# Performance work log

Hardware: AMD Instinct MI355X
Metric: run time of the kernel (lower is better)

Reference implementation:

```python
import jax, jax.numpy as jnp
import numpy as np

B, S, D, H = 2, 2048, 1024, 16
DK = D // H


def setup_inputs() -> dict:
    key = jax.random.key(0)
    ks = jax.random.split(key, 12)
    lim = 1.0 / np.sqrt(D)
    def lin(kw, kb):
        W = jax.random.uniform(kw, (D, D), jnp.float32, -lim, lim)
        b = jax.random.uniform(kb, (D,), jnp.float32, -lim, lim)
        return W, b
    Wq, bq = lin(ks[0], ks[1])
    Wk, bk = lin(ks[2], ks[3])
    Wv, bv = lin(ks[4], ks[5])
    Wo, bo = lin(ks[6], ks[7])
    Q = jax.random.normal(ks[8], (B, S, D), jnp.float32)
    K = jax.random.normal(ks[9], (B, S, D), jnp.float32)
    V = jax.random.normal(ks[10], (B, S, D), jnp.float32)
    # causal mask, broadcastable to (B, H, S, S)
    mask = jnp.broadcast_to(jnp.tril(jnp.ones((S, S), jnp.bool_))[None, None], (B, 1, S, S))
    return {"Q": Q, "K": K, "V": V, "mask": mask,
            "Wq": Wq, "bq": bq, "Wk": Wk, "bk": bk,
            "Wv": Wv, "bv": bv, "Wo": Wo, "bo": bo}


def reference(Q, K, V, mask, Wq, bq, Wk, bk, Wv, bv, Wo, bo):
    def split(x):  # (B,S,D) -> (B,H,S,DK)
        return x.reshape(B, S, H, DK).transpose(0, 2, 1, 3)
    q = split(Q @ Wq.T + bq)
    k = split(K @ Wk.T + bk)
    v = split(V @ Wv.T + bv)
    scores = jnp.einsum('bhqd,bhkd->bhqk', q, k) / jnp.sqrt(jnp.float32(DK))
    scores = jnp.where(mask, scores, jnp.float32(-1e9))
    probs = jax.nn.softmax(scores, axis=-1)
    out = jnp.einsum('bhqk,bhkd->bhqd', probs, v)  # (B,H,S,DK)
    out = out.transpose(0, 2, 1, 3).reshape(B, S, D)
    return out @ Wo.T + bo
```

## Files before the change

### kernel.cpp

```cpp
#include <hip/hip_runtime.h>

#define S_LEN 2048
#define D_DIM 1024
#define H_NUM 16
#define DK_DIM 64
#define BATCH 2
#define M_TOT (BATCH * S_LEN)

typedef __bf16 bf16x8 __attribute__((ext_vector_type(8)));
typedef float f32x4 __attribute__((ext_vector_type(4)));
typedef unsigned short u16;

__device__ inline u16 f2bf(float f) {
  union { float f; unsigned u; } v; v.f = f;
  unsigned u = v.u;
  return (u16)((u + 0x7FFFu + ((u >> 16) & 1u)) >> 16);
}

__global__ __launch_bounds__(256)
void proj_kernel(const float* __restrict__ Q, const float* __restrict__ K,
                 const float* __restrict__ V,
                 const float* __restrict__ Wq, const float* __restrict__ bq,
                 const float* __restrict__ Wk, const float* __restrict__ bk,
                 const float* __restrict__ Wv, const float* __restrict__ bv,
                 u16* __restrict__ qh, u16* __restrict__ kh,
                 u16* __restrict__ vt) {
  const int z = blockIdx.z;
  const float* X    = (z == 0) ? Q  : (z == 1) ? K  : V;
  const float* W    = (z == 0) ? Wq : (z == 1) ? Wk : Wv;
  const float* bias = (z == 0) ? bq : (z == 1) ? bk : bv;
  u16* out          = (z == 0) ? qh : (z == 1) ? kh : vt;

  __shared__ __align__(16) u16 Asm[128][40];
  __shared__ __align__(16) u16 Bsm[128][40];

  const int tid  = threadIdx.x;
  const int m0   = blockIdx.x * 128;
  const int n0   = blockIdx.y * 128;
  const int wid  = tid >> 6;
  const int lane = tid & 63;
  const int col  = lane & 15;
  const int quad = lane >> 4;
  const int wm   = (wid >> 1) * 64;
  const int wn   = (wid & 1) * 64;

  f32x4 acc[4][4];
  const f32x4 zero4 = {0.f, 0.f, 0.f, 0.f};
  for (int i = 0; i < 4; i++)
    for (int j = 0; j < 4; j++) acc[i][j] = zero4;

  const int sr = tid >> 3;
  const int sc = (tid & 7) * 4;

  for (int k0 = 0; k0 < D_DIM; k0 += 32) {
    __syncthreads();
    for (int p = 0; p < 4; p++) {
      const int row = p * 32 + sr;
      const float4 av = *reinterpret_cast<const float4*>(
          &X[(size_t)(m0 + row) * D_DIM + k0 + sc]);
      ushort4 aw;
      aw.x = f2bf(av.x); aw.y = f2bf(av.y); aw.z = f2bf(av.z); aw.w = f2bf(av.w);
      *reinterpret_cast<ushort4*>(&Asm[row][sc]) = aw;
      const float4 bvv = *reinterpret_cast<const float4*>(
          &W[(size_t)(n0 + row) * D_DIM + k0 + sc]);
      ushort4 bw;
      bw.x = f2bf(bvv.x); bw.y = f2bf(bvv.y); bw.z = f2bf(bvv.z); bw.w = f2bf(bvv.w);
      *reinterpret_cast<ushort4*>(&Bsm[row][sc]) = bw;
    }
    __syncthreads();

    bf16x8 af[4], bfm[4];
    for (int i = 0; i < 4; i++)
      af[i] = *reinterpret_cast<const bf16x8*>(&Asm[wm + i * 16 + col][quad * 8]);
    for (int j = 0; j < 4; j++)
      bfm[j] = *reinterpret_cast<const bf16x8*>(&Bsm[wn + j * 16 + col][quad * 8]);
    for (int i = 0; i < 4; i++)
      for (int j = 0; j < 4; j++)
        acc[i][j] = __builtin_amdgcn_mfma_f32_16x16x32_bf16(af[i], bfm[j],
                                                            acc[i][j], 0, 0, 0);
  }

  for (int i = 0; i < 4; i++) {
    const int gm_base = m0 + wm + i * 16 + quad * 4;
    for (int j = 0; j < 4; j++) {
      const int gn = n0 + wn + j * 16 + col;
      const float bb = bias[gn];
      const int h = gn >> 6, dk = gn & 63;
      for (int r = 0; r < 4; r++) {
        const int token = gm_base + r;
        const int b = token >> 11, s = token & (S_LEN - 1);
        const float val = acc[i][j][r] + bb;
        size_t idx;
        if (z == 2)
          idx = ((size_t)(b * H_NUM + h) * DK_DIM + dk) * S_LEN + s;
        else
          idx = ((size_t)(b * H_NUM + h) * S_LEN + s) * DK_DIM + dk;
        out[idx] = f2bf(val);
      }
    }
  }
}

#define SCALE_LOG2 0.18033688f

__global__ __launch_bounds__(256)
void attn_kernel(const u16* __restrict__ qh, const u16* __restrict__ kh,
                 const u16* __restrict__ vt, u16* __restrict__ ctx) {
  __shared__ __align__(16) u16 Ksm[64][72];
  __shared__ __align__(16) u16 Vsm[64][72];
  __shared__ __align__(16) u16 Psm[4][32][72];

  const int tid  = threadIdx.x;
  const int bh   = blockIdx.y;
  const int qb   = (blockIdx.y & 16) ? (15 - blockIdx.x) : blockIdx.x;
  const int q0   = qb * 128;
  const int wid  = tid >> 6;
  const int lane = tid & 63;
  const int col  = lane & 15;
  const int quad = lane >> 4;
  const int qrow_w = q0 + wid * 32;

  bf16x8 qB[2][2];
  for (int ss = 0; ss < 2; ss++) {
    const u16* qp =
        &qh[((size_t)bh * S_LEN + qrow_w + ss * 16 + col) * DK_DIM + quad * 8];
    qB[ss][0] = *reinterpret_cast<const bf16x8*>(qp);
    qB[ss][1] = *reinterpret_cast<const bf16x8*>(qp + 32);
  }

  float m_[2] = {-INFINITY, -INFINITY};
  float l_[2] = {0.f, 0.f};
  f32x4 o[4][2];
  const f32x4 zero4 = {0.f, 0.f, 0.f, 0.f};
  for (int dm = 0; dm < 4; dm++)
    for (int ss = 0; ss < 2; ss++) o[dm][ss] = zero4;

  const int ntiles = qb * 2 + 2;
  const int sr = tid >> 2;
  const int sc = (tid & 3) * 8;

  for (int t = 0; t < ntiles; t++) {
    const int kv0 = t * 64;
    __syncthreads();
    {
      const u16* kp = &kh[((size_t)bh * S_LEN + kv0 + sr) * DK_DIM + sc];
      *reinterpret_cast<uint4*>(&Ksm[sr][sc]) =
          *reinterpret_cast<const uint4*>(kp);
      *reinterpret_cast<uint4*>(&Ksm[sr][sc + 32]) =
          *reinterpret_cast<const uint4*>(kp + 32);
      const u16* vp = &vt[((size_t)bh * DK_DIM + sr) * S_LEN + kv0 + sc];
      *reinterpret_cast<uint4*>(&Vsm[sr][sc]) =
          *reinterpret_cast<const uint4*>(vp);
      *reinterpret_cast<uint4*>(&Vsm[sr][sc + 32]) =
          *reinterpret_cast<const uint4*>(vp + 32);
    }
    __syncthreads();

    bf16x8 kA[4][2];
    for (int nc = 0; nc < 4; nc++) {
      kA[nc][0] = *reinterpret_cast<const bf16x8*>(&Ksm[nc * 16 + col][quad * 8]);
      kA[nc][1] =
          *reinterpret_cast<const bf16x8*>(&Ksm[nc * 16 + col][32 + quad * 8]);
    }

    for (int ss = 0; ss < 2; ss++) {
      const int qrs = qrow_w + ss * 16;
      const int qg  = qrs + col;
      f32x4 s[4];
      for (int nc = 0; nc < 4; nc++) {
        f32x4 acc = zero4;
        acc = __builtin_amdgcn_mfma_f32_16x16x32_bf16(kA[nc][0], qB[ss][0],
                                                      acc, 0, 0, 0);
        acc = __builtin_amdgcn_mfma_f32_16x16x32_bf16(kA[nc][1], qB[ss][1],
                                                      acc, 0, 0, 0);
        s[nc] = acc;
      }
      float x[4][4];
      const bool domask = (kv0 + 63 > qrs);
      for (int nc = 0; nc < 4; nc++)
        for (int r = 0; r < 4; r++) {
          float v = s[nc][r] * SCALE_LOG2;
          if (domask && (kv0 + nc * 16 + quad * 4 + r > qg)) v = -INFINITY;
          x[nc][r] = v;
        }
      float tm = x[0][0];
      for (int nc = 0; nc < 4; nc++)
        for (int r = 0; r < 4; r++) tm = fmaxf(tm, x[nc][r]);
      tm = fmaxf(tm, __shfl_xor(tm, 16));
      tm = fmaxf(tm, __shfl_xor(tm, 32));
      const float mn    = fmaxf(m_[ss], tm);
      const float alpha = __builtin_amdgcn_exp2f(m_[ss] - mn);
      m_[ss] = mn;
      float rs = 0.f;
      ushort4 pk[4];
      for (int nc = 0; nc < 4; nc++) {
        float p0 = __builtin_amdgcn_exp2f(x[nc][0] - mn);
        float p1 = __builtin_amdgcn_exp2f(x[nc][1] - mn);
        float p2 = __builtin_amdgcn_exp2f(x[nc][2] - mn);
        float p3 = __builtin_amdgcn_exp2f(x[nc][3] - mn);
        rs += (p0 + p1) + (p2 + p3);
        pk[nc].x = f2bf(p0); pk[nc].y = f2bf(p1);
        pk[nc].z = f2bf(p2); pk[nc].w = f2bf(p3);
      }
      rs += __shfl_xor(rs, 16);
      rs += __shfl_xor(rs, 32);
      l_[ss] = l_[ss] * alpha + rs;
      for (int dm = 0; dm < 4; dm++) o[dm][ss] *= alpha;
      for (int nc = 0; nc < 4; nc++)
        *reinterpret_cast<ushort4*>(
            &Psm[wid][ss * 16 + col][nc * 16 + quad * 4]) = pk[nc];
    }

    asm volatile("s_waitcnt lgkmcnt(0)" ::: "memory");

    bf16x8 pB[2][2];
    for (int ss = 0; ss < 2; ss++) {
      pB[0][ss] = *reinterpret_cast<const bf16x8*>(
          &Psm[wid][ss * 16 + col][quad * 8]);
      pB[1][ss] = *reinterpret_cast<const bf16x8*>(
          &Psm[wid][ss * 16 + col][32 + quad * 8]);
    }
    for (int dm = 0; dm < 4; dm++) {
      const bf16x8 vA0 =
          *reinterpret_cast<const bf16x8*>(&Vsm[dm * 16 + col][quad * 8]);
      const bf16x8 vA1 =
          *reinterpret_cast<const bf16x8*>(&Vsm[dm * 16 + col][32 + quad * 8]);
      for (int ss = 0; ss < 2; ss++) {
        o[dm][ss] = __builtin_amdgcn_mfma_f32_16x16x32_bf16(vA0, pB[0][ss],
                                                            o[dm][ss], 0, 0, 0);
        o[dm][ss] = __builtin_amdgcn_mfma_f32_16x16x32_bf16(vA1, pB[1][ss],
                                                            o[dm][ss], 0, 0, 0);
      }
    }
  }

  const int b = bh >> 4, h = bh & 15;
  for (int ss = 0; ss < 2; ss++) {
    const float inv = 1.0f / l_[ss];
    const int qg = qrow_w + ss * 16 + col;
    for (int dm = 0; dm < 4; dm++) {
      ushort4 w;
      w.x = f2bf(o[dm][ss][0] * inv);
      w.y = f2bf(o[dm][ss][1] * inv);
      w.z = f2bf(o[dm][ss][2] * inv);
      w.w = f2bf(o[dm][ss][3] * inv);
      *reinterpret_cast<ushort4*>(
          &ctx[((size_t)b * S_LEN + qg) * D_DIM + h * DK_DIM + dm * 16 +
               quad * 4]) = w;
    }
  }
}

__global__ __launch_bounds__(256)
void outproj_kernel(const u16* __restrict__ ctx, const float* __restrict__ Wo,
                    const float* __restrict__ bo, float* __restrict__ out) {
  __shared__ __align__(16) u16 Asm[128][40];
  __shared__ __align__(16) u16 Bsm[128][40];

  const int tid  = threadIdx.x;
  const int m0   = blockIdx.x * 128;
  const int n0   = blockIdx.y * 128;
  const int wid  = tid >> 6;
  const int lane = tid & 63;
  const int col  = lane & 15;
  const int quad = lane >> 4;
  const int wm   = (wid >> 1) * 64;
  const int wn   = (wid & 1) * 64;

  f32x4 acc[4][4];
  const f32x4 zero4 = {0.f, 0.f, 0.f, 0.f};
  for (int i = 0; i < 4; i++)
    for (int j = 0; j < 4; j++) acc[i][j] = zero4;

  const int ar = tid >> 2, ac = (tid & 3) * 8;
  const int sr = tid >> 3, sc = (tid & 7) * 4;

  for (int k0 = 0; k0 < D_DIM; k0 += 32) {
    __syncthreads();
    for (int p = 0; p < 2; p++) {
      const int row = p * 64 + ar;
      *reinterpret_cast<uint4*>(&Asm[row][ac]) =
          *reinterpret_cast<const uint4*>(&ctx[(size_t)(m0 + row) * D_DIM + k0 + ac]);
    }
    for (int p = 0; p < 4; p++) {
      const int row = p * 32 + sr;
      const float4 bvv = *reinterpret_cast<const float4*>(
          &Wo[(size_t)(n0 + row) * D_DIM + k0 + sc]);
      ushort4 bw;
      bw.x = f2bf(bvv.x); bw.y = f2bf(bvv.y); bw.z = f2bf(bvv.z); bw.w = f2bf(bvv.w);
      *reinterpret_cast<ushort4*>(&Bsm[row][sc]) = bw;
    }
    __syncthreads();

    bf16x8 af[4], bfm[4];
    for (int i = 0; i < 4; i++)
      af[i] = *reinterpret_cast<const bf16x8*>(&Asm[wm + i * 16 + col][quad * 8]);
    for (int j = 0; j < 4; j++)
      bfm[j] = *reinterpret_cast<const bf16x8*>(&Bsm[wn + j * 16 + col][quad * 8]);
    for (int i = 0; i < 4; i++)
      for (int j = 0; j < 4; j++)
        acc[i][j] = __builtin_amdgcn_mfma_f32_16x16x32_bf16(af[i], bfm[j],
                                                            acc[i][j], 0, 0, 0);
  }

  for (int i = 0; i < 4; i++) {
    const int gm_base = m0 + wm + i * 16 + quad * 4;
    for (int j = 0; j < 4; j++) {
      const int gn = n0 + wn + j * 16 + col;
      const float bb = bo[gn];
      for (int r = 0; r < 4; r++) {
        const int token = gm_base + r;
        out[(size_t)token * D_DIM + gn] = acc[i][j][r] + bb;
      }
    }
  }
}

extern "C" void kernel_launch(void* const* d_in, const int* in_sizes, int n_in,
                              void* d_out, int out_size, void* d_ws,
                              size_t ws_size, hipStream_t stream) {
  const float* Q  = (const float*)d_in[0];
  const float* K  = (const float*)d_in[1];
  const float* V  = (const float*)d_in[2];
  const float* Wq = (const float*)d_in[4];
  const float* bq = (const float*)d_in[5];
  const float* Wk = (const float*)d_in[6];
  const float* bk = (const float*)d_in[7];
  const float* Wv = (const float*)d_in[8];
  const float* bv = (const float*)d_in[9];
  const float* Wo = (const float*)d_in[10];
  const float* bo = (const float*)d_in[11];
  float* out = (float*)d_out;

  const size_t NE = (size_t)BATCH * H_NUM * S_LEN * DK_DIM;
  u16* qh  = (u16*)d_ws;
  u16* kh  = qh + NE;
  u16* vt  = kh + NE;
  u16* ctx = vt + NE;

  proj_kernel<<<dim3(M_TOT / 128, D_DIM / 128, 3), 256, 0, stream>>>(
      Q, K, V, Wq, bq, Wk, bk, Wv, bv, qh, kh, vt);
  attn_kernel<<<dim3(S_LEN / 128, BATCH * H_NUM), 256, 0, stream>>>(qh, kh, vt,
                                                                    ctx);
  outproj_kernel<<<dim3(M_TOT / 128, D_DIM / 128), 256, 0, stream>>>(ctx, Wo,
                                                                     bo, out);
}
```

Measured before the change: 290.9 us.

## Pre-convert inputs to bf16 and use direct-to-LDS loads in projection GEMMs

Adds a separate conversion kernel that casts Q/K/V and all four weight matrices to bf16 once, so the GEMMs no longer convert fp32 per tile. The projection and output GEMMs become one templated kernel. It loads tiles with global_load_lds into an XOR-swizzled 64-wide K tile, swaps MFMA operand order where needed so stores can be vectorized, and writes ushort4/float4 epilogues. This trades an extra full pass over the inputs and extra workspace for cheaper, wider GEMM staging with fewer syncs per K step.

After: 266.4 us. 8.4% less time.

```diff
diff --git a/kernel.cpp b/kernel.cpp
--- a/kernel.cpp
+++ b/kernel.cpp
@@ -6,6 +6,8 @@
 #define DK_DIM 64
 #define BATCH 2
 #define M_TOT (BATCH * S_LEN)
+#define XSZ 4194304
+#define WSZ 1048576
 
 typedef __bf16 bf16x8 __attribute__((ext_vector_type(8)));
 typedef float f32x4 __attribute__((ext_vector_type(4)));
@@ -17,85 +19,161 @@
   return (u16)((u + 0x7FFFu + ((u >> 16) & 1u)) >> 16);
 }
 
+typedef const __attribute__((address_space(1))) unsigned int gu32;
+typedef __attribute__((address_space(3))) unsigned int lu32;
+__device__ inline void glds16(const u16* g, u16* l) {
+  __builtin_amdgcn_global_load_lds((gu32*)g, (lu32*)l, 16, 0, 0);
+}
+
 __global__ __launch_bounds__(256)
-void proj_kernel(const float* __restrict__ Q, const float* __restrict__ K,
-                 const float* __restrict__ V,
-                 const float* __restrict__ Wq, const float* __restrict__ bq,
-                 const float* __restrict__ Wk, const float* __restrict__ bk,
-                 const float* __restrict__ Wv, const float* __restrict__ bv,
-                 u16* __restrict__ qh, u16* __restrict__ kh,
-                 u16* __restrict__ vt) {
-  const int z = blockIdx.z;
-  const float* X    = (z == 0) ? Q  : (z == 1) ? K  : V;
-  const float* W    = (z == 0) ? Wq : (z == 1) ? Wk : Wv;
-  const float* bias = (z == 0) ? bq : (z == 1) ? bk : bv;
-  u16* out          = (z == 0) ? qh : (z == 1) ? kh : vt;
-
-  __shared__ __align__(16) u16 Asm[128][40];
-  __shared__ __align__(16) u16 Bsm[128][40];
-
-  const int tid  = threadIdx.x;
-  const int m0   = blockIdx.x * 128;
-  const int n0   = blockIdx.y * 128;
-  const int wid  = tid >> 6;
-  const int lane = tid & 63;
-  const int col  = lane & 15;
-  const int quad = lane >> 4;
-  const int wm   = (wid >> 1) * 64;
-  const int wn   = (wid & 1) * 64;
+void convert_kernel(const float* __restrict__ Q, const float* __restrict__ K,
+                    const float* __restrict__ V, const float* __restrict__ Wq,
+                    const float* __restrict__ Wk, const float* __restrict__ Wv,
+                    const float* __restrict__ Wo, u16* __restrict__ Xb,
+                    u16* __restrict__ Wb) {
+  const size_t e = ((size_t)blockIdx.x * 256 + threadIdx.x) * 8;
+  const float* src;
+  u16* dst;
+  size_t off;
+  if (e < 3ull * XSZ) {
+    const int a = (int)(e >> 22);
+    src = (a == 0) ? Q : (a == 1) ? K : V;
+    off = e - ((size_t)a << 22);
+    dst = Xb + e;
+  } else {
+    const size_t ew = e - 3ull * XSZ;
+    const int a = (int)(ew >> 20);
+    src = (a == 0) ? Wq : (a == 1) ? Wk : (a == 2) ? Wv : Wo;
+    off = ew - ((size_t)a << 20);
+    dst = Wb + ew;
+  }
+  const float4 v0 = *reinterpret_cast<const float4*>(&src[off]);
+  const float4 v1 = *reinterpret_cast<const float4*>(&src[off + 4]);
+  ushort4 w0, w1;
+  w0.x = f2bf(v0.x); w0.y = f2bf(v0.y); w0.z = f2bf(v0.z); w0.w = f2bf(v0.w);
+  w1.x = f2bf(v1.x); w1.y = f2bf(v1.y); w1.z = f2bf(v1.z); w1.w = f2bf(v1.w);
+  *reinterpret_cast<ushort4*>(dst) = w0;
+  *reinterpret_cast<ushort4*>(dst + 4) = w1;
+}
+
+template <int MODE>
+__global__ __launch_bounds__(256)
+void gemm_kernel(const u16* __restrict__ A0, const u16* __restrict__ B0,
+                 const float* __restrict__ bias0, void* __restrict__ out0,
+                 const u16* __restrict__ A1, const u16* __restrict__ B1,
+                 const float* __restrict__ bias1, void* __restrict__ out1) {
+  const u16* A = A0;
+  const u16* Bw = B0;
+  const float* bias = bias0;
+  void* outp = out0;
+  if (MODE == 0 && blockIdx.z == 1) { A = A1; Bw = B1; bias = bias1; outp = out1; }
+
+  __shared__ __align__(16) u16 Asm[128 * 64];
+  __shared__ __align__(16) u16 Bsm[128 * 64];
+
+  const int tid = threadIdx.x;
+  const int m0 = blockIdx.x * 128, n0 = blockIdx.y * 128;
+  const int wid = tid >> 6, lane = tid & 63;
+  const int col = lane & 15, quad = lane >> 4;
+  const int wm = (wid >> 1) * 64, wn = (wid & 1) * 64;
+
+  const int lr = lane >> 3;
+  const int lc = (lane & 7) ^ lr;
+  const u16* gA = A + (size_t)(m0 + 32 * wid + lr) * D_DIM + lc * 8;
+  const u16* gB = Bw + (size_t)(n0 + 32 * wid + lr) * D_DIM + lc * 8;
 
   f32x4 acc[4][4];
   const f32x4 zero4 = {0.f, 0.f, 0.f, 0.f};
   for (int i = 0; i < 4; i++)
     for (int j = 0; j < 4; j++) acc[i][j] = zero4;
 
-  const int sr = tid >> 3;
-  const int sc = (tid & 7) * 4;
-
-  for (int k0 = 0; k0 < D_DIM; k0 += 32) {
+  for (int k0 = 0; k0 < D_DIM; k0 += 64) {
     __syncthreads();
-    for (int p = 0; p < 4; p++) {
-      const int row = p * 32 + sr;
-      const float4 av = *reinterpret_cast<const float4*>(
-          &X[(size_t)(m0 + row) * D_DIM + k0 + sc]);
-      ushort4 aw;
-      aw.x = f2bf(av.x); aw.y = f2bf(av.y); aw.z = f2bf(av.z); aw.w = f2bf(av.w);
-      *reinterpret_cast<ushort4*>(&Asm[row][sc]) = aw;
-      const float4 bvv = *reinterpret_cast<const float4*>(
-          &W[(size_t)(n0 + row) * D_DIM + k0 + sc]);
-      ushort4 bw;
-      bw.x = f2bf(bvv.x); bw.y = f2bf(bvv.y); bw.z = f2bf(bvv.z); bw.w = f2bf(bvv.w);
-      *reinterpret_cast<ushort4*>(&Bsm[row][sc]) = bw;
+    for (int j = 0; j < 4; j++) {
+      glds16(gA + (size_t)j * 8 * D_DIM + k0, &Asm[(32 * wid + 8 * j) * 64]);
+      glds16(gB + (size_t)j * 8 * D_DIM + k0, &Bsm[(32 * wid + 8 * j) * 64]);
     }
     __syncthreads();
 
-    bf16x8 af[4], bfm[4];
-    for (int i = 0; i < 4; i++)
-      af[i] = *reinterpret_cast<const bf16x8*>(&Asm[wm + i * 16 + col][quad * 8]);
+    bf16x8 af[4][2], bfm[4][2];
+    for (int i = 0; i < 4; i++) {
+      const int row = wm + i * 16 + col;
+      const int r7 = row & 7;
+      af[i][0] = *reinterpret_cast<const bf16x8*>(&Asm[row * 64 + ((quad ^ r7) * 8)]);
+      af[i][1] = *reinterpret_cast<const bf16x8*>(&Asm[row * 64 + (((quad + 4) ^ r7) * 8)]);
+    }
+    for (int j = 0; j < 4; j++) {
+      const int row = wn + j * 16 + col;
+      const int r7 = row & 7;
+      bfm[j][0] = *reinterpret_cast<const bf16x8*>(&Bsm[row * 64 + ((quad ^ r7) * 8)]);
+      bfm[j][1] = *reinterpret_cast<const bf16x8*>(&Bsm[row * 64 + (((quad + 4) ^ r7) * 8)]);
+    }
+    for (int h = 0; h < 2; h++)
+      for (int i = 0; i < 4; i++)
+        for (int j = 0; j < 4; j++) {
+          if (MODE == 1)
+            acc[i][j] = __builtin_amdgcn_mfma_f32_16x16x32_bf16(
+                af[i][h], bfm[j][h], acc[i][j], 0, 0, 0);
+          else
+            acc[i][j] = __builtin_amdgcn_mfma_f32_16x16x32_bf16(
+                bfm[j][h], af[i][h], acc[i][j], 0, 0, 0);
+        }
+  }
+
+  if (MODE == 0) {
+    u16* out = (u16*)outp;
+    float4 b4[4];
     for (int j = 0; j < 4; j++)
-      bfm[j] = *reinterpret_cast<const bf16x8*>(&Bsm[wn + j * 16 + col][quad * 8]);
-    for (int i = 0; i < 4; i++)
-      for (int j = 0; j < 4; j++)
-        acc[i][j] = __builtin_amdgcn_mfma_f32_16x16x32_bf16(af[i], bfm[j],
-                                                            acc[i][j], 0, 0, 0);
-  }
-
-  for (int i = 0; i < 4; i++) {
-    const int gm_base = m0 + wm + i * 16 + quad * 4;
-    for (int j = 0; j < 4; j++) {
-      const int gn = n0 + wn + j * 16 + col;
-      const float bb = bias[gn];
-      const int h = gn >> 6, dk = gn & 63;
-      for (int r = 0; r < 4; r++) {
-        const int token = gm_base + r;
-        const int b = token >> 11, s = token & (S_LEN - 1);
-        const float val = acc[i][j][r] + bb;
-        size_t idx;
-        if (z == 2)
-          idx = ((size_t)(b * H_NUM + h) * DK_DIM + dk) * S_LEN + s;
-        else
-          idx = ((size_t)(b * H_NUM + h) * S_LEN + s) * DK_DIM + dk;
-        out[idx] = f2bf(val);
+      b4[j] = *reinterpret_cast<const float4*>(&bias[n0 + wn + j * 16 + quad * 4]);
+    for (int i = 0; i < 4; i++) {
+      const int token = m0 + wm + i * 16 + col;
+      const int b = token >> 11, s = token & (S_LEN - 1);
+      for (int j = 0; j < 4; j++) {
+        const int gnb = n0 + wn + j * 16 + quad * 4;
+        const int h = gnb >> 6, dk = gnb & 63;
+        ushort4 w;
+        w.x = f2bf(acc[i][j][0] + b4[j].x);
+        w.y = f2bf(acc[i][j][1] + b4[j].y);
+        w.z = f2bf(acc[i][j][2] + b4[j].z);
+        w.w = f2bf(acc[i][j][3] + b4[j].w);
+        *reinterpret_cast<ushort4*>(
+            &out[((size_t)(b * H_NUM + h) * S_LEN + s) * DK_DIM + dk]) = w;
+      }
+    }
+  } else if (MODE == 1) {
+    u16* out = (u16*)outp;
+    float bb[4];
+    for (int j = 0; j < 4; j++) bb[j] = bias[n0 + wn + j * 16 + col];
+    for (int i = 0; i < 4; i++) {
+      const int token0 = m0 + wm + i * 16 + quad * 4;
+      const int b = token0 >> 11, s0 = token0 & (S_LEN - 1);
+      for (int j = 0; j < 4; j++) {
+        const int gn = n0 + wn + j * 16 + col;
+        const int h = gn >> 6, dk = gn & 63;
+        ushort4 w;
+        w.x = f2bf(acc[i][j][0] + bb[j]);
+        w.y = f2bf(acc[i][j][1] + bb[j]);
+        w.z = f2bf(acc[i][j][2] + bb[j]);
+        w.w = f2bf(acc[i][j][3] + bb[j]);
+        *reinterpret_cast<ushort4*>(
+            &out[((size_t)(b * H_NUM + h) * DK_DIM + dk) * S_LEN + s0]) = w;
+      }
+    }
+  } else {
+    float* out = (float*)outp;
+    float4 b4[4];
+    for (int j = 0; j < 4; j++)
+      b4[j] = *reinterpret_cast<const float4*>(&bias[n0 + wn + j * 16 + quad * 4]);
+    for (int i = 0; i < 4; i++) {
+      const int token = m0 + wm + i * 16 + col;
+      for (int j = 0; j < 4; j++) {
+        const int gnb = n0 + wn + j * 16 + quad * 4;
+        float4 v;
+        v.x = acc[i][j][0] + b4[j].x;
+        v.y = acc[i][j][1] + b4[j].y;
+        v.z = acc[i][j][2] + b4[j].z;
+        v.w = acc[i][j][3] + b4[j].w;
+        *reinterpret_cast<float4*>(&out[(size_t)token * D_DIM + gnb]) = v;
       }
     }
   }
@@ -251,71 +329,6 @@
   }
 }
 
-__global__ __launch_bounds__(256)
-void outproj_kernel(const u16* __restrict__ ctx, const float* __restrict__ Wo,
-                    const float* __restrict__ bo, float* __restrict__ out) {
-  __shared__ __align__(16) u16 Asm[128][40];
-  __shared__ __align__(16) u16 Bsm[128][40];
-
-  const int tid  = threadIdx.x;
-  const int m0   = blockIdx.x * 128;
-  const int n0   = blockIdx.y * 128;
-  const int wid  = tid >> 6;
-  const int lane = tid & 63;
-  const int col  = lane & 15;
-  const int quad = lane >> 4;
-  const int wm   = (wid >> 1) * 64;
-  const int wn   = (wid & 1) * 64;
-
-  f32x4 acc[4][4];
-  const f32x4 zero4 = {0.f, 0.f, 0.f, 0.f};
-  for (int i = 0; i < 4; i++)
-    for (int j = 0; j < 4; j++) acc[i][j] = zero4;
-
-  const int ar = tid >> 2, ac = (tid & 3) * 8;
-  const int sr = tid >> 3, sc = (tid & 7) * 4;
-
-  for (int k0 = 0; k0 < D_DIM; k0 += 32) {
-    __syncthreads();
-    for (int p = 0; p < 2; p++) {
-      const int row = p * 64 + ar;
-      *reinterpret_cast<uint4*>(&Asm[row][ac]) =
-          *reinterpret_cast<const uint4*>(&ctx[(size_t)(m0 + row) * D_DIM + k0 + ac]);
-    }
-    for (int p = 0; p < 4; p++) {
-      const int row = p * 32 + sr;
-      const float4 bvv = *reinterpret_cast<const float4*>(
-          &Wo[(size_t)(n0 + row) * D_DIM + k0 + sc]);
-      ushort4 bw;
-      bw.x = f2bf(bvv.x); bw.y = f2bf(bvv.y); bw.z = f2bf(bvv.z); bw.w = f2bf(bvv.w);
-      *reinterpret_cast<ushort4*>(&Bsm[row][sc]) = bw;
-    }
-    __syncthreads();
-
-    bf16x8 af[4], bfm[4];
-    for (int i = 0; i < 4; i++)
-      af[i] = *reinterpret_cast<const bf16x8*>(&Asm[wm + i * 16 + col][quad * 8]);
-    for (int j = 0; j < 4; j++)
-      bfm[j] = *reinterpret_cast<const bf16x8*>(&Bsm[wn + j * 16 + col][quad * 8]);
-    for (int i = 0; i < 4; i++)
-      for (int j = 0; j < 4; j++)
-        acc[i][j] = __builtin_amdgcn_mfma_f32_16x16x32_bf16(af[i], bfm[j],
-                                                            acc[i][j], 0, 0, 0);
-  }
-
-  for (int i = 0; i < 4; i++) {
-    const int gm_base = m0 + wm + i * 16 + quad * 4;
-    for (int j = 0; j < 4; j++) {
-      const int gn = n0 + wn + j * 16 + col;
-      const float bb = bo[gn];
-      for (int r = 0; r < 4; r++) {
-        const int token = gm_base + r;
-        out[(size_t)token * D_DIM + gn] = acc[i][j][r] + bb;
-      }
-    }
-  }
-}
-
 extern "C" void kernel_launch(void* const* d_in, const int* in_sizes, int n_in,
                               void* d_out, int out_size, void* d_ws,
                               size_t ws_size, hipStream_t stream) {
@@ -332,16 +345,29 @@
   const float* bo = (const float*)d_in[11];
   float* out = (float*)d_out;
 
-  const size_t NE = (size_t)BATCH * H_NUM * S_LEN * DK_DIM;
   u16* qh  = (u16*)d_ws;
-  u16* kh  = qh + NE;
-  u16* vt  = kh + NE;
-  u16* ctx = vt + NE;
-
-  proj_kernel<<<dim3(M_TOT / 128, D_DIM / 128, 3), 256, 0, stream>>>(
-      Q, K, V, Wq, bq, Wk, bk, Wv, bv, qh, kh, vt);
+  u16* kh  = qh + XSZ;
+  u16* vt  = kh + XSZ;
+  u16* Qb  = vt + XSZ;
+  u16* ctx = Qb;
+  u16* Kb  = Qb + XSZ;
+  u16* Vb  = Kb + XSZ;
+  u16* Wqb = Vb + XSZ;
+  u16* Wkb = Wqb + WSZ;
+  u16* Wvb = Wkb + WSZ;
+  u16* Wob = Wvb + WSZ;
+
+  convert_kernel<<<(3 * XSZ + 4 * WSZ) / (256 * 8), 256, 0, stream>>>(
+      Q, K, V, Wq, Wk, Wv, Wo, Qb, Wqb);
+
+  gemm_kernel<0><<<dim3(M_TOT / 128, D_DIM / 128, 2), 256, 0, stream>>>(
+      Qb, Wqb, bq, qh, Kb, Wkb, bk, kh);
+  gemm_kernel<1><<<dim3(M_TOT / 128, D_DIM / 128, 1), 256, 0, stream>>>(
+      Vb, Wvb, bv, vt, nullptr, nullptr, nullptr, nullptr);
+
   attn_kernel<<<dim3(S_LEN / 128, BATCH * H_NUM), 256, 0, stream>>>(qh, kh, vt,
                                                                     ctx);
-  outproj_kernel<<<dim3(M_TOT / 128, D_DIM / 128), 256, 0, stream>>>(ctx, Wo,
-                                                                     bo, out);
-}
+
+  gemm_kernel<2><<<dim3(M_TOT / 128, D_DIM / 128, 1), 256, 0, stream>>>(
+      ctx, Wob, bo, out, nullptr, nullptr, nullptr, nullptr);
+}
```
